# Kernel tuning notes

Measured on AMD Instinct MI355X. Metric: run time of the kernel, lower is better.

Reference implementation:

```python
import jax, jax.numpy as jnp
import numpy as np

P = 7      # pool_size
R = 128    # num_rois
KB = 8     # static max bin extent = floor(wh_max / P) = floor(56/7)


def setup_inputs() -> dict:
    key = jax.random.key(0)
    k1, k2, k3 = jax.random.split(key, 3)
    x = jax.random.normal(k1, (1, 256, 64, 64), dtype=jnp.float32)
    xy = jax.random.randint(k2, (R, 2), 0, 8)            # top-left corners
    wh = jax.random.randint(k3, (R, 2), P, 57)           # w,h in [7,56]: every bin non-empty
    rois = jnp.concatenate([xy, wh], axis=1).astype(jnp.int32)  # [R,4] = (x,y,w,h)
    return {"x": x, "rois": rois}


def _bin_indices(coord, size, limit):
    # Replicates: x1 = int(x + ix*rl); x2 = int(x1 + rl); clamp to [0, limit].
    rl = size.astype(jnp.float32) / P                                    # [R]
    starts = jnp.floor(coord[:, None].astype(jnp.float32)
                       + jnp.arange(P, dtype=jnp.float32) * rl[:, None]).astype(jnp.int32)  # [R,P]
    ends = starts + jnp.floor(rl).astype(jnp.int32)[:, None]             # [R,P]
    starts = jnp.maximum(starts, 0)
    ends = jnp.minimum(ends, limit)
    idx = starts[:, :, None] + jnp.arange(KB, dtype=jnp.int32)           # [R,P,KB]
    valid = idx < ends[:, :, None]
    return jnp.clip(idx, 0, limit - 1), valid


def reference(x, rois):
    B, C, H, W = x.shape
    NEG = jnp.finfo(x.dtype).min
    idx_x, val_x = _bin_indices(rois[:, 0], rois[:, 2], W)   # [R,P,KB]
    idx_y, val_y = _bin_indices(rois[:, 1], rois[:, 3], H)   # [R,P,KB]

    def pool_one(iy, vy, ix, vx):
        # iy,ix: [P,KB] row/col indices for this roi's bins; vy,vx: validity masks
        g = jnp.where(vy[None, None, :, :, None], x[:, :, iy, :], NEG).max(axis=3)  # [B,C,P,W]
        g = jnp.where(vx[None, None, None, :, :], g[:, :, :, ix], NEG).max(axis=4)  # [B,C,Py,Px]
        return g

    out = jax.vmap(pool_one)(idx_y, val_y, idx_x, val_x)     # [R,B,C,P,P]
    # torch: view(-1, num_rois, P, P, C).permute(0,1,4,2,3) -> [1, R, C, P, P] (valid for B=1)
    return out.transpose(1, 0, 2, 3, 4)
```

## Files before the change

### kernel.cpp

```cpp
#include <hip/hip_runtime.h>

#define R 128
#define C 256
#define P 7
#define HW 64
#define SROW 68
#define SLAB (4 * P * SROW + 8)

__global__ __launch_bounds__(256) void
roi_pool_kernel(const float* __restrict__ x,
                const int* __restrict__ rois,
                float* __restrict__ out) {
    const int lane = threadIdx.x & 63;
    const int wid  = __builtin_amdgcn_readfirstlane(threadIdx.x >> 6);
    const int gw   = blockIdx.x * 4 + wid;
    const int cq = gw & 63;
    const int r  = gw >> 6;
    const int c0 = cq << 2;

    __shared__ float vmbuf[4][SLAB];
    float* slab = vmbuf[wid];

    const int rx = rois[r * 4 + 0];
    const int ry = rois[r * 4 + 1];
    const int rw = rois[r * 4 + 2];
    const int rh = rois[r * 4 + 3];

    const float rlx = (float)rw / 7.0f;
    const float rly = (float)rh / 7.0f;
    const int kw = __builtin_amdgcn_readfirstlane((int)rlx);
    const int kh = __builtin_amdgcn_readfirstlane((int)rly);

    const int syv = (int)floorf(__fadd_rn((float)ry, __fmul_rn((float)lane, rly)));
    const int sy0 = __builtin_amdgcn_readlane(syv, 0);
    const int sy1 = __builtin_amdgcn_readlane(syv, 1);
    const int sy2 = __builtin_amdgcn_readlane(syv, 2);
    const int sy3 = __builtin_amdgcn_readlane(syv, 3);
    const int sy4 = __builtin_amdgcn_readlane(syv, 4);
    const int sy5 = __builtin_amdgcn_readlane(syv, 5);
    const int sy6 = __builtin_amdgcn_readlane(syv, 6);

    const int ch = lane >> 4;
    const int g  = lane & 15;
    const float* xch = x + ((size_t)(c0 + ch) << 12) + (g << 2);
    const float NEG = -3.402823466e38f;
    const float4 NEG4 = make_float4(NEG, NEG, NEG, NEG);

#define MAX4(a, b) make_float4(fmaxf((a).x,(b).x), fmaxf((a).y,(b).y), \
                               fmaxf((a).z,(b).z), fmaxf((a).w,(b).w))

#define BAND(PY, SY, KH)                                                      \
    {                                                                         \
        const float4* p = (const float4*)(xch + (SY) * HW);                   \
        float4 v[KH];                                                         \
        _Pragma("unroll")                                                     \
        for (int j = 0; j < KH; ++j) v[j] = p[j * 16];                        \
        float4 m = v[0];                      \
        _Pragma("unroll")                                                     \
        for (int j = 1; j < KH; ++j) {                                        \
            float4 t = (j < kh) ? v[j] : NEG4;                                \
            m = MAX4(m, t);                                                   \
        }                                                                     \
        *(float4*)(&slab[(ch * P + (PY)) * SROW + (g << 2)]) = m;             \
    }

    if (kh <= 4) {
        BAND(0,sy0,4) BAND(1,sy1,4) BAND(2,sy2,4) BAND(3,sy3,4)
        BAND(4,sy4,4) BAND(5,sy5,4) BAND(6,sy6,4)
    } else {
        BAND(0,sy0,8) BAND(1,sy1,8) BAND(2,sy2,8) BAND(3,sy3,8)
        BAND(4,sy4,8) BAND(5,sy5,8) BAND(6,sy6,8)
    }
#undef BAND

    if (lane < P * P) {
        const int py = lane / 7;
        const int px = lane - py * 7;
        const int sx = (int)floorf(__fadd_rn((float)rx, __fmul_rn((float)px, rlx)));
        const float* wp = slab + py * SROW + sx;
        const size_t obase = ((size_t)(r << 8) + c0) * (P * P) + lane;

        #pragma unroll
        for (int cc = 0; cc < 4; ++cc) {
            const float* w = wp + cc * (P * SROW);
            float m;
            if (kw <= 4) {
                float a0 = w[0], a1 = w[1], a2 = w[2], a3 = w[3];
                m = a0;
                m = fmaxf(m, (1 < kw) ? a1 : NEG);
                m = fmaxf(m, (2 < kw) ? a2 : NEG);
                m = fmaxf(m, (3 < kw) ? a3 : NEG);
            } else {
                float a0 = w[0], a1 = w[1], a2 = w[2], a3 = w[3];
                float a4 = w[4], a5 = w[5], a6 = w[6], a7 = w[7];
                m = fmaxf(fmaxf(fmaxf(a0, a1), fmaxf(a2, a3)), a4);
                m = fmaxf(m, (5 < kw) ? a5 : NEG);
                m = fmaxf(m, (6 < kw) ? a6 : NEG);
                m = fmaxf(m, (7 < kw) ? a7 : NEG);
            }
            out[obase + cc * (P * P)] = m;
        }
    }
}

extern "C" void kernel_launch(void* const* d_in, const int* in_sizes, int n_in,
                              void* d_out, int out_size, void* d_ws, size_t ws_size,
                              hipStream_t stream) {
    const float* x = (const float*)d_in[0];
    const int* rois = (const int*)d_in[1];
    float* out = (float*)d_out;

    const int grid = (R * C / 4) / 4;
    roi_pool_kernel<<<grid, 256, 0, stream>>>(x, rois, out);
}
```

Baseline: 18.89 us.

## Process two channels per wavefront with float2 loads instead of four

```diff
diff --git a/kernel.cpp b/kernel.cpp
--- a/kernel.cpp
+++ b/kernel.cpp
@@ -4,8 +4,8 @@
 #define C 256
 #define P 7
 #define HW 64
-#define SROW 68
-#define SLAB (4 * P * SROW + 8)
+#define SW 72
+#define CHSLAB (P * SW)
 
 __global__ __launch_bounds__(256) void
 roi_pool_kernel(const float* __restrict__ x,
@@ -14,11 +14,10 @@
     const int lane = threadIdx.x & 63;
     const int wid  = __builtin_amdgcn_readfirstlane(threadIdx.x >> 6);
     const int gw   = blockIdx.x * 4 + wid;
-    const int cq = gw & 63;
-    const int r  = gw >> 6;
-    const int c0 = cq << 2;
+    const int cp = gw & 127;
+    const int r  = gw >> 7;
 
-    __shared__ float vmbuf[4][SLAB];
+    __shared__ float vmbuf[4][2 * CHSLAB];
     float* slab = vmbuf[wid];
 
     const int rx = rois[r * 4 + 0];
@@ -40,28 +39,28 @@
     const int sy5 = __builtin_amdgcn_readlane(syv, 5);
     const int sy6 = __builtin_amdgcn_readlane(syv, 6);
 
-    const int ch = lane >> 4;
-    const int g  = lane & 15;
-    const float* xch = x + ((size_t)(c0 + ch) << 12) + (g << 2);
+    const int half = lane >> 5;
+    const int g    = lane & 31;
+    const float* base = x + ((size_t)((cp << 1) + half) << 12) + (g << 1);
+
     const float NEG = -3.402823466e38f;
-    const float4 NEG4 = make_float4(NEG, NEG, NEG, NEG);
+    const float2 NEG2 = make_float2(NEG, NEG);
 
-#define MAX4(a, b) make_float4(fmaxf((a).x,(b).x), fmaxf((a).y,(b).y), \
-                               fmaxf((a).z,(b).z), fmaxf((a).w,(b).w))
+#define MAX2(a, b) make_float2(fmaxf((a).x,(b).x), fmaxf((a).y,(b).y))
 
 #define BAND(PY, SY, KH)                                                      \
     {                                                                         \
-        const float4* p = (const float4*)(xch + (SY) * HW);                   \
-        float4 v[KH];                                                         \
+        const float* p = base + (SY) * HW;                                    \
+        float2 v[KH];                                                         \
         _Pragma("unroll")                                                     \
-        for (int j = 0; j < KH; ++j) v[j] = p[j * 16];                        \
-        float4 m = v[0];                      \
+        for (int j = 0; j < KH; ++j) v[j] = *(const float2*)(p + j * HW);     \
+        float2 m = v[0];                                         \
         _Pragma("unroll")                                                     \
         for (int j = 1; j < KH; ++j) {                                        \
-            float4 t = (j < kh) ? v[j] : NEG4;                                \
-            m = MAX4(m, t);                                                   \
+            float2 t = (j < kh) ? v[j] : NEG2;                                \
+            m = MAX2(m, t);                                                   \
         }                                                                     \
-        *(float4*)(&slab[(ch * P + (PY)) * SROW + (g << 2)]) = m;             \
+        *(float2*)(&slab[half * CHSLAB + (PY) * SW + (g << 1)]) = m;          \
     }
 
     if (kh <= 4) {
@@ -77,12 +76,11 @@
         const int py = lane / 7;
         const int px = lane - py * 7;
         const int sx = (int)floorf(__fadd_rn((float)rx, __fmul_rn((float)px, rlx)));
-        const float* wp = slab + py * SROW + sx;
-        const size_t obase = ((size_t)(r << 8) + c0) * (P * P) + lane;
+        const size_t obase = ((size_t)(r << 8) + (cp << 1)) * (P * P) + lane;
 
         #pragma unroll
-        for (int cc = 0; cc < 4; ++cc) {
-            const float* w = wp + cc * (P * SROW);
+        for (int cc = 0; cc < 2; ++cc) {
+            const float* w = slab + cc * CHSLAB + py * SW + sx;
             float m;
             if (kw <= 4) {
                 float a0 = w[0], a1 = w[1], a2 = w[2], a3 = w[3];
@@ -110,6 +108,6 @@
     const int* rois = (const int*)d_in[1];
     float* out = (float*)d_out;
 
-    const int grid = (R * C / 4) / 4;
+    const int grid = (R * C / 2) / 4;
     roi_pool_kernel<<<grid, 256, 0, stream>>>(x, rois, out);
 }
```

After: 27.32 us. 44.6% more time.
